# Performance work log

Hardware: AMD Instinct MI355X
Metric: run time of the kernel (lower is better)

## Reference

```python
import jax, jax.numpy as jnp
import numpy as np


def setup_inputs() -> dict:
    key = jax.random.key(0)
    k1, k2 = jax.random.split(key)
    B, N, M = 4, 8192, 8192
    xyz1 = jax.random.normal(k1, (B, N, 3), dtype=jnp.float32)
    xyz2 = jax.random.normal(k2, (B, M, 3), dtype=jnp.float32)
    th = jnp.float32(0.1)
    return {"xyz1": xyz1, "xyz2": xyz2, "th": th}


def reference(xyz1, xyz2, th):
    # Pairwise squared distances (B, N, M) via the expanded form
    x2 = jnp.sum(xyz1 * xyz1, axis=-1)                    # (B, N)
    y2 = jnp.sum(xyz2 * xyz2, axis=-1)                    # (B, M)
    cross = jnp.einsum('bnd,bmd->bnm', xyz1, xyz2)        # (B, N, M)
    dist = x2[:, :, None] + y2[:, None, :] - 2.0 * cross  # (B, N, M)
    # torch: distances is (B, M, N); min over dim=1 -> per-x min (our axis=2),
    #        min over dim=2 -> per-y min (our axis=1).
    d1 = jnp.min(dist, axis=2)                            # (B, N)
    d2 = jnp.min(dist, axis=1)                            # (B, M)
    d1 = jnp.where(d1 <= th, jnp.float32(0.0), d1)
    d2 = jnp.where(d2 <= th, jnp.float32(0.0), d2)
    return jnp.mean(d1, axis=1) + jnp.mean(d2, axis=1)    # (B,)
```

## Files before the change

kernel.cpp:

```cpp
#include <hip/hip_runtime.h>
#include <math.h>

#define NBATCH 4
#define NPTS   8192
#define TPB    512
#define NWAVE  (TPB / 64)
#define QPT    16
#define QPAIRS (QPT / 2)
#define QPB    (64 * QPT)
#define QTILES (NPTS / QPB)
#define PSPLIT 8
#define PPB    (NPTS / PSPLIT)
#define SLICE  (PPB / NWAVE)
#define NBLK   (2 * NBATCH * QTILES * PSPLIT)
#define NTILEB (2 * NBATCH * QTILES)

typedef float v2f __attribute__((ext_vector_type(2)));
typedef float v4f __attribute__((ext_vector_type(4)));

__device__ __forceinline__ float min3f(float a, float b, float c) {
    return fminf(fminf(a, b), c);
}

__global__ __launch_bounds__(TPB, 4) void chamfer_main(
    const float* __restrict__ xyz1,
    const float* __restrict__ xyz2,
    float* __restrict__ ws_part)
{
    __shared__ float sx[PPB] __attribute__((aligned(16)));
    __shared__ float sy[PPB] __attribute__((aligned(16)));
    __shared__ float sz[PPB] __attribute__((aligned(16)));
    __shared__ float sw[PPB] __attribute__((aligned(16)));
    __shared__ float part[NWAVE][QPB];

    const int bid  = blockIdx.x;
    const int ps   = bid & (PSPLIT - 1);
    const int r1   = bid >> 3;
    const int tile = r1 & (QTILES - 1);
    const int r2   = r1 >> 3;
    const int b    = r2 & (NBATCH - 1);
    const int dir  = r2 >> 2;

    const float* q  = (dir == 0 ? xyz1 : xyz2) + (size_t)b * NPTS * 3;
    const float* rp = (dir == 0 ? xyz2 : xyz1) + (size_t)b * NPTS * 3
                      + (size_t)ps * PPB * 3;

    for (int i = threadIdx.x; i < PPB; i += TPB) {
        float x = rp[3 * i + 0], y = rp[3 * i + 1], z = rp[3 * i + 2];
        sx[i] = -2.0f * x;
        sy[i] = -2.0f * y;
        sz[i] = -2.0f * z;
        sw[i] = x * x + y * y + z * z;
    }
    __syncthreads();

    const int lane = threadIdx.x & 63;
    const int w    = threadIdx.x >> 6;
    const int q0   = tile * QPB + lane * QPT;

    v2f qx2[QPAIRS], qy2[QPAIRS], qz2[QPAIRS];
    float m[QPT];
    #pragma unroll
    for (int p = 0; p < QPAIRS; ++p) {
        const int iA = q0 + 2 * p, iB = iA + 1;
        qx2[p] = (v2f){ q[3 * iA + 0], q[3 * iB + 0] };
        qy2[p] = (v2f){ q[3 * iA + 1], q[3 * iB + 1] };
        qz2[p] = (v2f){ q[3 * iA + 2], q[3 * iB + 2] };
        m[2 * p] = INFINITY;
        m[2 * p + 1] = INFINITY;
    }

    const int base = w * SLICE;
    #pragma unroll 1
    for (int j = 0; j < SLICE; j += 8) {
        v4f X0 = *(const v4f*)&sx[base + j];
        v4f X1 = *(const v4f*)&sx[base + j + 4];
        v4f Y0 = *(const v4f*)&sy[base + j];
        v4f Y1 = *(const v4f*)&sy[base + j + 4];
        v4f Z0 = *(const v4f*)&sz[base + j];
        v4f Z1 = *(const v4f*)&sz[base + j + 4];
        v4f W0 = *(const v4f*)&sw[base + j];
        v4f W1 = *(const v4f*)&sw[base + j + 4];

        v2f Px[4] = { X0.lo, X0.hi, X1.lo, X1.hi };
        v2f Py[4] = { Y0.lo, Y0.hi, Y1.lo, Y1.hi };
        v2f Pz[4] = { Z0.lo, Z0.hi, Z1.lo, Z1.hi };
        v2f Pw[4] = { W0.lo, W0.hi, W1.lo, W1.hi };

        #pragma unroll
        for (int g = 0; g < 4; ++g) {
            const v2f xs = __builtin_shufflevector(Px[g], Px[g], 1, 0);
            const v2f ys = __builtin_shufflevector(Py[g], Py[g], 1, 0);
            const v2f zs = __builtin_shufflevector(Pz[g], Pz[g], 1, 0);
            const v2f wsw = __builtin_shufflevector(Pw[g], Pw[g], 1, 0);
            #pragma unroll
            for (int p = 0; p < QPAIRS; ++p) {
                v2f c1 = __builtin_elementwise_fma(qx2[p], Px[g],
                         __builtin_elementwise_fma(qy2[p], Py[g],
                         __builtin_elementwise_fma(qz2[p], Pz[g], Pw[g])));
                v2f c2 = __builtin_elementwise_fma(qx2[p], xs,
                         __builtin_elementwise_fma(qy2[p], ys,
                         __builtin_elementwise_fma(qz2[p], zs, wsw)));
                m[2 * p]     = min3f(m[2 * p],     c1.x, c2.x);
                m[2 * p + 1] = min3f(m[2 * p + 1], c1.y, c2.y);
            }
        }
    }

    #pragma unroll
    for (int k = 0; k < QPT; ++k) {
        const int col = lane * QPT + ((k + lane) & (QPT - 1));
        part[w][col] = m[k];
    }
    __syncthreads();

    for (int ql = threadIdx.x; ql < QPB; ql += TPB) {
        const int l   = ql >> 4;
        const int col = (ql & ~(QPT - 1)) | ((ql + l) & (QPT - 1));
        float mv = part[0][col];
        #pragma unroll
        for (int s = 1; s < NWAVE; ++s) mv = fminf(mv, part[s][col]);
        const int qi = tile * QPB + ql;
        const float Qx = q[3 * qi + 0], Qy = q[3 * qi + 1], Qz = q[3 * qi + 2];
        ws_part[(size_t)bid * QPB + ql] = (Qx * Qx + Qy * Qy + Qz * Qz) + mv;
    }
}

__global__ __launch_bounds__(256) void chamfer_finalize1(
    const float* __restrict__ ws_part,
    const float* __restrict__ thp,
    double* __restrict__ tile_sums)
{
    __shared__ double wsum[4];
    const int t = blockIdx.x;
    const float th = *thp;
    const size_t gb = (size_t)t * PSPLIT;
    double acc = 0.0;
    for (int ql = threadIdx.x; ql < QPB; ql += 256) {
        float mv = ws_part[(gb + 0) * QPB + ql];
        #pragma unroll
        for (int s = 1; s < PSPLIT; ++s)
            mv = fminf(mv, ws_part[(gb + s) * QPB + ql]);
        acc += (mv <= th) ? 0.0 : (double)mv;
    }
    for (int off = 32; off > 0; off >>= 1)
        acc += __shfl_down(acc, off, 64);
    const int lane = threadIdx.x & 63;
    const int w    = threadIdx.x >> 6;
    if (lane == 0) wsum[w] = acc;
    __syncthreads();
    if (threadIdx.x == 0) {
        double s = wsum[0] + wsum[1] + wsum[2] + wsum[3];
        tile_sums[t] = s;
    }
}

__global__ void chamfer_finalize2(const double* __restrict__ tile_sums,
                                  float* __restrict__ out)
{
    const int b = threadIdx.x;
    if (b < NBATCH) {
        double s = 0.0;
        for (int dir = 0; dir < 2; ++dir)
            for (int t = 0; t < QTILES; ++t)
                s += tile_sums[(dir * NBATCH + b) * QTILES + t];
        out[b] = (float)(s / (double)NPTS);
    }
}

extern "C" void kernel_launch(void* const* d_in, const int* in_sizes, int n_in,
                              void* d_out, int out_size, void* d_ws, size_t ws_size,
                              hipStream_t stream) {
    const float* xyz1 = (const float*)d_in[0];
    const float* xyz2 = (const float*)d_in[1];
    const float* thp  = (const float*)d_in[2];
    float* out        = (float*)d_out;
    float* ws_part    = (float*)d_ws;
    double* tile_sums = (double*)(ws_part + NBLK * QPB);

    chamfer_main<<<NBLK, TPB, 0, stream>>>(xyz1, xyz2, ws_part);
    chamfer_finalize1<<<NTILEB, 256, 0, stream>>>(ws_part, thp, tile_sums);
    chamfer_finalize2<<<1, 64, 0, stream>>>(tile_sums, out);
}
```

Before: 49.16 us.

## Broadcast query coordinates into packed FMAs and halve the reference-point split

The inner loop now duplicates each query coordinate into both lanes of a packed float pair and pairs it with two consecutive reference points. This replaces the previous scheme of pairing two queries against swapped point pairs, so the per-group shuffles go away. The per-query min now uses an inline-asm v_min3_f32, and the reference split drops from 8 to 4, which halves the block count and the partial results written to the workspace. Launch bounds are relaxed to 2 blocks per CU to fit the larger register footprint of the duplicated query vectors. The risks are lower occupancy, and inline asm limiting the compiler's scheduling.

New measurement: 49.99 us. Within noise of the previous version (+1.7%).

```diff
diff --git a/kernel.cpp b/kernel.cpp
--- a/kernel.cpp
+++ b/kernel.cpp
@@ -6,10 +6,9 @@
 #define TPB    512
 #define NWAVE  (TPB / 64)
 #define QPT    16
-#define QPAIRS (QPT / 2)
 #define QPB    (64 * QPT)
 #define QTILES (NPTS / QPB)
-#define PSPLIT 8
+#define PSPLIT 4
 #define PPB    (NPTS / PSPLIT)
 #define SLICE  (PPB / NWAVE)
 #define NBLK   (2 * NBATCH * QTILES * PSPLIT)
@@ -18,11 +17,13 @@
 typedef float v2f __attribute__((ext_vector_type(2)));
 typedef float v4f __attribute__((ext_vector_type(4)));
 
-__device__ __forceinline__ float min3f(float a, float b, float c) {
-    return fminf(fminf(a, b), c);
+__device__ __forceinline__ float min3a(float m, float a, float b) {
+    float r;
+    asm("v_min3_f32 %0, %1, %2, %3" : "=v"(r) : "v"(m), "v"(a), "v"(b));
+    return r;
 }
 
-__global__ __launch_bounds__(TPB, 4) void chamfer_main(
+__global__ __launch_bounds__(TPB, 2) void chamfer_main(
     const float* __restrict__ xyz1,
     const float* __restrict__ xyz2,
     float* __restrict__ ws_part)
@@ -35,7 +36,7 @@
 
     const int bid  = blockIdx.x;
     const int ps   = bid & (PSPLIT - 1);
-    const int r1   = bid >> 3;
+    const int r1   = bid >> 2;
     const int tile = r1 & (QTILES - 1);
     const int r2   = r1 >> 3;
     const int b    = r2 & (NBATCH - 1);
@@ -58,16 +59,17 @@
     const int w    = threadIdx.x >> 6;
     const int q0   = tile * QPB + lane * QPT;
 
-    v2f qx2[QPAIRS], qy2[QPAIRS], qz2[QPAIRS];
+    v2f qxv[QPT], qyv[QPT], qzv[QPT];
     float m[QPT];
     #pragma unroll
-    for (int p = 0; p < QPAIRS; ++p) {
-        const int iA = q0 + 2 * p, iB = iA + 1;
-        qx2[p] = (v2f){ q[3 * iA + 0], q[3 * iB + 0] };
-        qy2[p] = (v2f){ q[3 * iA + 1], q[3 * iB + 1] };
-        qz2[p] = (v2f){ q[3 * iA + 2], q[3 * iB + 2] };
-        m[2 * p] = INFINITY;
-        m[2 * p + 1] = INFINITY;
+    for (int k = 0; k < QPT; ++k) {
+        const float Qx = q[3 * (q0 + k) + 0];
+        const float Qy = q[3 * (q0 + k) + 1];
+        const float Qz = q[3 * (q0 + k) + 2];
+        qxv[k] = (v2f){ Qx, Qx };
+        qyv[k] = (v2f){ Qy, Qy };
+        qzv[k] = (v2f){ Qz, Qz };
+        m[k]   = INFINITY;
     }
 
     const int base = w * SLICE;
@@ -89,20 +91,12 @@
 
         #pragma unroll
         for (int g = 0; g < 4; ++g) {
-            const v2f xs = __builtin_shufflevector(Px[g], Px[g], 1, 0);
-            const v2f ys = __builtin_shufflevector(Py[g], Py[g], 1, 0);
-            const v2f zs = __builtin_shufflevector(Pz[g], Pz[g], 1, 0);
-            const v2f wsw = __builtin_shufflevector(Pw[g], Pw[g], 1, 0);
             #pragma unroll
-            for (int p = 0; p < QPAIRS; ++p) {
-                v2f c1 = __builtin_elementwise_fma(qx2[p], Px[g],
-                         __builtin_elementwise_fma(qy2[p], Py[g],
-                         __builtin_elementwise_fma(qz2[p], Pz[g], Pw[g])));
-                v2f c2 = __builtin_elementwise_fma(qx2[p], xs,
-                         __builtin_elementwise_fma(qy2[p], ys,
-                         __builtin_elementwise_fma(qz2[p], zs, wsw)));
-                m[2 * p]     = min3f(m[2 * p],     c1.x, c2.x);
-                m[2 * p + 1] = min3f(m[2 * p + 1], c1.y, c2.y);
+            for (int k = 0; k < QPT; ++k) {
+                v2f d = __builtin_elementwise_fma(qxv[k], Px[g],
+                        __builtin_elementwise_fma(qyv[k], Py[g],
+                        __builtin_elementwise_fma(qzv[k], Pz[g], Pw[g])));
+                m[k] = min3a(m[k], d.x, d.y);
             }
         }
     }
@@ -150,8 +144,7 @@
     if (lane == 0) wsum[w] = acc;
     __syncthreads();
     if (threadIdx.x == 0) {
-        double s = wsum[0] + wsum[1] + wsum[2] + wsum[3];
-        tile_sums[t] = s;
+        tile_sums[t] = wsum[0] + wsum[1] + wsum[2] + wsum[3];
     }
 }
 
```
